# Optimization experiments

Measured on AMD Instinct MI355X. Metric: run time of the kernel, lower is better.

The kernel has to match this reference:

```python
import jax, jax.numpy as jnp
import numpy as np
from jax import lax

GROUPS = 8            # _resolve_groups(256, 8) == 8
EPS = 1e-5            # GroupNorm default eps
TOPK_RATIO = 0.2
MEAN_W, TOPK_W = 0.7, 0.3
DMG_THRESH = 0.5
DN = ('NCHW', 'OIHW', 'NCHW')


def _normalize(p, axis=1):
    # clamp_min(1e-8) / clamp_min(1e-8).sum().clamp_min(1e-8)
    p = jnp.maximum(p, 1e-8)
    return p / jnp.maximum(p.sum(axis=axis, keepdims=True), 1e-8)


def _conv_head(x, w1, gn_s, gn_b, w2, b2):
    # Conv3x3(no bias) -> GroupNorm(8) -> GELU(exact) -> Dropout(eval: identity) -> Conv1x1
    h = lax.conv_general_dilated(x, w1, (1, 1), 'SAME', dimension_numbers=DN)
    B, C, H, W = h.shape
    hg = h.reshape(B, GROUPS, C // GROUPS, H, W)
    mu = jnp.mean(hg, axis=(2, 3, 4), keepdims=True)
    var = jnp.var(hg, axis=(2, 3, 4), keepdims=True)
    h = ((hg - mu) * lax.rsqrt(var + EPS)).reshape(B, C, H, W)
    h = h * gn_s[None, :, None, None] + gn_b[None, :, None, None]
    h = jax.nn.gelu(h, approximate=False)
    return lax.conv_general_dilated(h, w2, (1, 1), 'SAME', dimension_numbers=DN) + b2[None, :, None, None]


def _forward(feature_map, target_mask, dw1, dgs, dgb, dw2, db2, sw1, sgs, sgb, sw2, sb2):
    dmg_logit = _conv_head(feature_map, dw1, dgs, dgb, dw2, db2)      # [B,1,H,W]
    corn_logits = _conv_head(feature_map, sw1, sgs, sgb, sw2, sb2)    # [B,2,H,W]

    # CORN dense decode: threshold probs = cumprod(sigmoid), classes = K+1
    t = jnp.cumprod(jax.nn.sigmoid(corn_logits), axis=1)              # [B,2,H,W]
    sev = jnp.concatenate([1.0 - t[:, :1], t[:, :-1] - t[:, 1:], t[:, -1:]], axis=1)  # [B,3,H,W]
    sev = _normalize(sev, axis=1)

    p_dmg = jax.nn.sigmoid(dmg_logit)                                 # [B,1,H,W]
    pix = jnp.concatenate([1.0 - p_dmg, p_dmg * sev], axis=1)         # [B,4,H,W]
    pix = _normalize(pix, axis=1)

    sev_pred = jnp.argmax(sev, axis=1) + 1                            # [B,H,W]
    pred_labels = jnp.where(p_dmg[:, 0] >= DMG_THRESH, sev_pred, 0)

    # target_mask already at feature resolution -> nearest resize is identity
    valid = target_mask > 0.5                                         # [B,1,H,W] bool
    B, C, H, W = pix.shape
    N = H * W
    flat = pix.transpose(0, 2, 3, 1).reshape(B, N, C)                 # [B,N,C]
    mf = valid.reshape(B, N)                                          # [B,N]
    cnt = mf.sum(axis=1)                                              # [B] int
    uniform = jnp.full((B, C), 1.0 / C, dtype=flat.dtype)

    # masked mean
    denom = jnp.maximum(cnt, 1).astype(flat.dtype)[:, None]
    mean_p = (flat * mf[..., None]).sum(axis=1) / denom
    mean_p = jnp.where((cnt == 0)[:, None], uniform, mean_p)
    mean_p = _normalize(mean_p, axis=1)

    # masked top-k mean via descending sort + cumsum gather (probs >= 0, invalid -> -1)
    masked = jnp.where(mf[..., None], flat, jnp.asarray(-1.0, flat.dtype))
    srt = -jnp.sort(-masked, axis=1)                                  # descending [B,N,C]
    csum = jnp.cumsum(srt, axis=1)
    k = jnp.clip(jnp.round(cnt.astype(jnp.float32) * TOPK_RATIO).astype(jnp.int32), 1, jnp.maximum(cnt, 1))
    idx = jnp.broadcast_to((k - 1)[:, None, None], (B, 1, C))
    topk_p = jnp.take_along_axis(csum, idx, axis=1)[:, 0] / k.astype(flat.dtype)[:, None]
    topk_p = jnp.where((cnt == 0)[:, None], uniform, topk_p)
    topk_p = _normalize(topk_p, axis=1)

    agg = _normalize(MEAN_W * mean_p + TOPK_W * topk_p, axis=1)
    agg_labels = jnp.argmax(agg, axis=1)

    return (dmg_logit, corn_logits, pix, pred_labels, mean_p, topk_p, agg, agg_labels)


def setup_inputs() -> dict:
    key = jax.random.key(0)
    ks = jax.random.split(key, 8)
    B, Cin, Ch, H, W = 8, 256, 256, 128, 128
    inp = {
        'feature_map': jax.random.normal(ks[0], (B, Cin, H, W), jnp.float32),
        'target_mask': jax.random.uniform(ks[1], (B, 1, H, W), jnp.float32),
        # damage head: Conv3x3 -> GN -> Conv1x1 (1 out)
        'dw1': jax.random.normal(ks[2], (Ch, Cin, 3, 3), jnp.float32) * 0.05,
        'dgs': jnp.ones((Ch,), jnp.float32),
        'dgb': jnp.zeros((Ch,), jnp.float32),
        'dw2': jax.random.normal(ks[3], (1, Ch, 1, 1), jnp.float32) * 0.05,
        'db2': jnp.zeros((1,), jnp.float32),
        # severity head: Conv3x3 -> GN -> Conv1x1 (2 thresholds)
        'sw1': jax.random.normal(ks[4], (Ch, Cin, 3, 3), jnp.float32) * 0.05,
        'sgs': jnp.ones((Ch,), jnp.float32),
        'sgb': jnp.zeros((Ch,), jnp.float32),
        'sw2': jax.random.normal(ks[5], (2, Ch, 1, 1), jnp.float32) * 0.05,
        'sb2': jnp.zeros((2,), jnp.float32),
    }
    return inp


def reference(feature_map, target_mask, dw1, dgs, dgb, dw2, db2, sw1, sgs, sgb, sw2, sb2):
    return _forward(feature_map, target_mask, dw1, dgs, dgb, dw2, db2, sw1, sgs, sgb, sw2, sb2)
```

## Files before the change

### kernel.cpp

```cpp
#include <hip/hip_runtime.h>
#include <hip/hip_bf16.h>

#define BB   8
#define CIN  256
#define CHN  256
#define HH   128
#define WWD  128
#define HW   (HH * WWD)
#define GRP_ELEMS ((size_t)32 * HW)

#define FLAG_DL   4e-3f
#define FLAG_GAP  1.5e-3f

#define BO_DSUM1   0
#define BO_DSUM2   1024
#define BO_FSTAT1  2048
#define BO_FSTAT2  2560
#define BO_DSTAT1  3072
#define BO_DSTAT2  4096
#define BO_MEAN    5120
#define BO_CNT     5248
#define BO_TOPK    5280
#define BO_FLAGC   5408
#define MEMSET_BYTES 8192
#define BO_WL      8192
#define WLCAP      32768

#define XP_OFF    139264ull
#define XP_BYTES  67108864ull
#define HB_OFF    (XP_OFF + XP_BYTES)
#define HB_BYTES  134217728ull
#define WH_OFF    (HB_OFF + HB_BYTES)
#define WT_BYTES  1179648ull
#define WL_OFF    (WH_OFF + WT_BYTES)
#define WT32_OFF  (WL_OFF + WT_BYTES)
#define WT32_BYTES 4718592ull
#define MFMA_NEED (WT32_OFF + WT32_BYTES)

#define O_DMG   0
#define O_CORN  131072
#define O_PIX   393216
#define O_LAB   917504
#define O_MEAN  1048576
#define O_TOPK  1048608
#define O_AGG   1048640
#define O_ALAB  1048672

typedef __attribute__((ext_vector_type(8))) _Float16 f16x8;
typedef __attribute__((ext_vector_type(4))) float f32x4;

__device__ inline ushort f2h(float f) {
    _Float16 h = (_Float16)f;
    union { _Float16 h; ushort u; } c; c.h = h; return c.u;
}
__device__ inline float h2f(ushort u) {
    union { ushort u; _Float16 h; } c; c.u = u; return (float)c.h;
}

__device__ inline void store4v(float* p, float a, float b, float c, float d) {
    *(float4*)p = make_float4(a, b, c, d);
}
__device__ inline void store4v(__hip_bfloat16* p, float a, float b, float c, float d) {
    p[0] = __float2bfloat16(a); p[1] = __float2bfloat16(b);
    p[2] = __float2bfloat16(c); p[3] = __float2bfloat16(d);
}
__device__ inline float ldv(const float* p) { return *p; }
__device__ inline float ldv(const __hip_bfloat16* p) { return __bfloat162float(*p); }


__global__ __launch_bounds__(256) void pack_x_f16(
    const float* __restrict__ x, ushort* __restrict__ Xh)
{
    int bid = blockIdx.x;
    int cc = bid & 7;
    int y  = (bid >> 3) & 127;
    int b  = bid >> 10;
    __shared__ ushort tile[32][132];
    for (int i = threadIdx.x; i < 4096; i += 256) {
        int ci = i >> 7, xx = i & 127;
        float v = x[(((size_t)b * 256 + cc * 32 + ci) * 128 + y) * 128 + xx];
        tile[ci][xx] = f2h(v);
    }
    __syncthreads();
    ushort* dst = Xh + ((((size_t)b * 128 + y) * 8 + cc) << 12);
    for (int i = threadIdx.x; i < 4096; i += 256) {
        int xx = i >> 5, ci = i & 31;
        dst[i] = tile[ci][xx];
    }
}

__global__ __launch_bounds__(256) void transpose_w(
    const float* __restrict__ w, ushort* __restrict__ Whh,
    ushort* __restrict__ Whl, float* __restrict__ Wt32)
{
    int idx = blockIdx.x * 256 + threadIdx.x;
    int tap = idx >> 16;
    int rem = idx & 65535;
    int cc  = rem >> 13;
    int co  = (rem >> 5) & 255;
    int ci5 = rem & 31;
    int ci  = cc * 32 + ci5;
    float v = w[((size_t)co * 256 + ci) * 9 + tap];
    ushort h = f2h(v);
    int sidx = (((tap * 8 + cc) * 16 + (co >> 4)) << 9)
             + (((co & 15) + ((ci5 >> 3) << 4)) << 3) + (ci5 & 7);
    Whh[sidx] = h;
    Whl[sidx] = f2h(v - h2f(h));
    Wt32[((size_t)tap * 256 + ci) * 256 + co] = v;
}

__device__ __forceinline__ void gld16(const void* g, void* l)
{
    __builtin_amdgcn_global_load_lds(
        (const __attribute__((address_space(1))) void*)g,
        (__attribute__((address_space(3))) void*)l, 16, 0, 0);
}

__device__ __forceinline__ void issue_b_slice(
    const ushort* __restrict__ Whh, const ushort* __restrict__ Whl,
    ushort* dst, int u, int co0, int tid, int wb)
{
    const int su  = u / 3;
    const int kxu = u - su * 3;
    const int tap = ((su >> 3) * 3) + kxu;
    const int cc  = su & 7;
    const size_t sbase = ((size_t)((tap * 8 + cc) * 16 + (co0 >> 4)) << 9);
    const ushort* s0 = Whh + sbase;
    const ushort* s1 = Whl + sbase;
#pragma unroll
    for (int k = 0; k < 2; k++)
        gld16(s0 + (k * 256 + tid) * 8, dst + (size_t)(k * 256 + wb) * 8);
#pragma unroll
    for (int k = 0; k < 2; k++)
        gld16(s1 + (k * 256 + tid) * 8, dst + 4096 + (size_t)(k * 256 + wb) * 8);
}

__device__ __forceinline__ void issue_a_slice(
    const ushort* __restrict__ Xh, const ushort* __restrict__ zb,
    ushort* dst, int b, int y, int sn, int tid, int wb)
{
    const int kyn = sn >> 3, ccn = sn & 7;
    const int rown = y + kyn - 1;
    const bool rv = (unsigned)rown < 128u;
    const ushort* base = rv ? (Xh + ((((size_t)b * 128 + rown) * 8 + ccn) << 12)) : zb;
#pragma unroll
    for (int k = 0; k < 2; k++) {
        int idx = k * 256 + tid;
        int xi  = (idx + 4) >> 2;
        int q   = (idx & 3) ^ ((xi >> 1) & 3);
        int off = rv ? ((xi - 1) * 32 + q * 8) : (idx * 8);
        gld16(base + off, dst + 32 + (size_t)(k * 256 + wb) * 8);
    }
}

__global__ __launch_bounds__(256, 3) void conv3x3_mfma(
    const ushort* __restrict__ Xh, const ushort* __restrict__ Whh,
    const ushort* __restrict__ Whl, const ushort* __restrict__ zb,
    float* __restrict__ hout, double* __restrict__ sums)
{
    __shared__ ushort a_lds[2][4160];
    __shared__ ushort b_lds[2][8192];
    __shared__ float sred[8];

    const int bx  = blockIdx.x;
    const int y   = bx & 127;
    const int b   = bx >> 7;
    const int co0 = blockIdx.y << 7;
    const int tid  = threadIdx.x;
    const int lane = tid & 63;
    const int wb   = tid & 192;
    const int wv   = tid >> 6;
    const int m = lane & 15;
    const int q = lane >> 4;
    const int wpx = (wv & 1) << 6;
    const int wco = (wv >> 1) << 6;
    const int g0  = wco >> 4;

    if (tid < 8) sred[tid] = 0.f;
    if (tid < 16) {
        int tg = tid >> 2, p4 = tid & 3;
        ushort* r = &a_lds[tg >> 1][(tg & 1) ? (129 * 32) : 0];
        *(uint4*)(r + p4 * 8) = make_uint4(0u, 0u, 0u, 0u);
    }

    f32x4 acc[4][4];
#pragma unroll
    for (int f = 0; f < 4; f++)
#pragma unroll
        for (int g = 0; g < 4; g++) acc[f][g] = (f32x4){0.f, 0.f, 0.f, 0.f};

    issue_a_slice(Xh, zb, a_lds[0], b, y, 0, tid, wb);
    issue_b_slice(Whh, Whl, b_lds[0], 0, co0, tid, wb);
    asm volatile("s_waitcnt lgkmcnt(0)" ::: "memory");

    for (int s = 0; s < 24; s++) {
        const ushort* acur = a_lds[s & 1];
#pragma unroll
        for (int kx = 0; kx < 3; kx++) {
            const int t = 3 * s + kx;
            asm volatile("" ::: "memory");
            __builtin_amdgcn_s_barrier();
            {
                int u = t + 1;
                int ub = u & 1;
                if (u > 71) u = 71;
                issue_b_slice(Whh, Whl, b_lds[ub], u, co0, tid, wb);
            }
            if (kx == 0) {
                int sn = s + 1;
                int ab = sn & 1;
                if (sn > 23) sn = 23;
                issue_a_slice(Xh, zb, a_lds[ab], b, y, sn, tid, wb);
            }
            if (kx == 2) asm volatile("s_waitcnt vmcnt(4)" ::: "memory");
            else         asm volatile("s_waitcnt vmcnt(6)" ::: "memory");
            __builtin_amdgcn_s_barrier();
            asm volatile("" ::: "memory");

            const ushort* bb = b_lds[t & 1];
            f16x8 ah[4], bh[4], bl[4];
#pragma unroll
            for (int f = 0; f < 4; f++) {
                int row = wpx + f * 16 + kx + m;
                ah[f] = *(const f16x8*)(acur + row * 32
                        + ((q ^ ((row >> 1) & 3)) << 3));
            }
#pragma unroll
            for (int g = 0; g < 4; g++) {
                int off = ((g0 + g) << 9) + (lane << 3);
                bh[g] = *(const f16x8*)&bb[off];
                bl[g] = *(const f16x8*)&bb[4096 + off];
            }
            __builtin_amdgcn_s_setprio(1);
#pragma unroll
            for (int f = 0; f < 4; f++)
#pragma unroll
                for (int g = 0; g < 4; g++)
                    acc[f][g] = __builtin_amdgcn_mfma_f32_16x16x32_f16(ah[f], bh[g], acc[f][g], 0, 0, 0);
#pragma unroll
            for (int f = 0; f < 4; f++)
#pragma unroll
                for (int g = 0; g < 4; g++)
                    acc[f][g] = __builtin_amdgcn_mfma_f32_16x16x32_f16(ah[f], bl[g], acc[f][g], 0, 0, 0);
            __builtin_amdgcn_s_setprio(0);
        }
    }

    float s0 = 0.f, q0 = 0.f, s1 = 0.f, q1 = 0.f;
#pragma unroll
    for (int f = 0; f < 4; f++) {
#pragma unroll
        for (int g = 0; g < 4; g++) {
            f32x4 v = acc[f][g];
            float a = v.x + v.y + v.z + v.w;
            float qq = v.x * v.x + v.y * v.y + v.z * v.z + v.w * v.w;
            if (g < 2) { s0 += a; q0 += qq; } else { s1 += a; q1 += qq; }
            int px = wpx + f * 16 + q * 4;
            int co = co0 + wco + g * 16 + m;
            *(f32x4*)&hout[((size_t)(b * 256 + co) * 128 + y) * 128 + px] = v;
        }
    }
    int gl = wco >> 5;
    atomicAdd(&sred[gl],     s0);
    atomicAdd(&sred[gl + 1], s1);
    atomicAdd(&sred[4 + gl],     q0);
    atomicAdd(&sred[4 + gl + 1], q1);
    __syncthreads();
    if (tid < 4) atomicAdd(&sums[b * 8 + (co0 >> 5) + tid], (double)sred[tid]);
    else if (tid < 8) atomicAdd(&sums[64 + b * 8 + (co0 >> 5) + tid - 4], (double)sred[tid]);
}

template <typename HT>
__global__ __launch_bounds__(256) void conv3x3_gn_stats(
    const float* __restrict__ x, const float* __restrict__ w,
    HT* __restrict__ hout, double* __restrict__ sums)
{
    __shared__ float in_lds[8][3][132];
    __shared__ float w_lds[8][9][68];
    __shared__ float sred[2], qred[2];

    const int bx  = blockIdx.x;
    const int y   = bx & (HH - 1);
    const int b   = bx >> 7;
    const int co0 = blockIdx.y << 6;
    const int tid = threadIdx.x;
    if (tid < 2) { sred[tid] = 0.f; qred[tid] = 0.f; }
    const int tco = (tid & 15) << 2;
    const int tox = (tid >> 4) << 3;

    float acc[4][8];
#pragma unroll
    for (int i = 0; i < 4; i++)
#pragma unroll
        for (int j = 0; j < 8; j++) acc[i][j] = 0.f;

    const float* xb = x + (size_t)b * CIN * HW;
    for (int c0 = 0; c0 < CIN; c0 += 8) {
        __syncthreads();
        for (int i = tid; i < 8 * 3 * 130; i += 256) {
            int ci  = i / 390;
            int rem = i - ci * 390;
            int r   = rem / 130;
            int cx  = rem - r * 130;
            int gy  = y + r - 1;
            int gx  = cx - 1;
            float v = 0.f;
            if ((unsigned)gy < HH && (unsigned)gx < WWD)
                v = xb[(size_t)(c0 + ci) * HW + gy * WWD + gx];
            in_lds[ci][r][cx] = v;
        }
        for (int i = tid; i < 64 * 72; i += 256) {
            int co = i / 72;
            int kk = i - co * 72;
            int ci = kk / 9;
            int k9 = kk - ci * 9;
            w_lds[ci][k9][co] = w[((size_t)(co0 + co) * CIN + (c0 + ci)) * 9 + k9];
        }
        __syncthreads();
#pragma unroll
        for (int ci = 0; ci < 8; ci++) {
#pragma unroll
            for (int ky = 0; ky < 3; ky++) {
                const float* rowp = &in_lds[ci][ky][tox];
                float4 a0 = *(const float4*)rowp;
                float4 a1 = *(const float4*)(rowp + 4);
                float2 a2 = *(const float2*)(rowp + 8);
                float in10[10] = {a0.x, a0.y, a0.z, a0.w,
                                  a1.x, a1.y, a1.z, a1.w, a2.x, a2.y};
#pragma unroll
                for (int kx = 0; kx < 3; kx++) {
                    float4 wv = *(const float4*)&w_lds[ci][ky * 3 + kx][tco];
#pragma unroll
                    for (int ox = 0; ox < 8; ox++) {
                        float iv = in10[ox + kx];
                        acc[0][ox] = fmaf(iv, wv.x, acc[0][ox]);
                        acc[1][ox] = fmaf(iv, wv.y, acc[1][ox]);
                        acc[2][ox] = fmaf(iv, wv.z, acc[2][ox]);
                        acc[3][ox] = fmaf(iv, wv.w, acc[3][ox]);
                    }
                }
            }
        }
    }

    float s = 0.f, qv = 0.f;
#pragma unroll
    for (int oc = 0; oc < 4; oc++)
#pragma unroll
        for (int ox = 0; ox < 8; ox++) { float v = acc[oc][ox]; s += v; qv = fmaf(v, v, qv); }
#pragma unroll
    for (int oc = 0; oc < 4; oc++) {
        size_t base = ((size_t)(b * CHN + co0 + tco + oc)) * HW + y * WWD + tox;
        store4v(hout + base,     acc[oc][0], acc[oc][1], acc[oc][2], acc[oc][3]);
        store4v(hout + base + 4, acc[oc][4], acc[oc][5], acc[oc][6], acc[oc][7]);
    }
    const int gsel = tco >> 5;
    atomicAdd(&sred[gsel], s);
    atomicAdd(&qred[gsel], qv);
    __syncthreads();
    if (tid < 2) {
        int grp = (co0 >> 5) + tid;
        atomicAdd(&sums[b * 8 + grp],      (double)sred[tid]);
        atomicAdd(&sums[64 + b * 8 + grp], (double)qred[tid]);
    }
}

__global__ void gn_finalize(const double* __restrict__ dsums,
                            float* __restrict__ fstats, double* __restrict__ dstats)
{
    int i = threadIdx.x;
    if (i < 64) {
        double inv = 1.0 / (double)GRP_ELEMS;
        double mu  = dsums[i] * inv;
        double ex2 = dsums[64 + i] * inv;
        double var = ex2 - mu * mu;
        double rs  = 1.0 / sqrt(var + 1e-5);
        fstats[i]      = (float)mu;
        fstats[64 + i] = (float)rs;
        dstats[i]      = mu;
        dstats[64 + i] = rs;
    }
}

template <typename HT>
__global__ __launch_bounds__(256) void gn_head(
    const HT* __restrict__ hbuf,
    const float* __restrict__ gs, const float* __restrict__ gb,
    const float* __restrict__ w2, const float* __restrict__ b2,
    const float* __restrict__ stats,
    float* __restrict__ out, int nout)
{
    __shared__ float sc[256], sh[256], w2s[2][256];
    const int b = blockIdx.y;
    const int p = blockIdx.x * 256 + threadIdx.x;
    {
        int c = threadIdx.x;
        float mu = stats[b * 8 + (c >> 5)];
        float rs = stats[64 + b * 8 + (c >> 5)];
        float s  = gs[c] * rs;
        sc[c] = s;
        sh[c] = gb[c] - mu * s;
        w2s[0][c] = w2[c];
        w2s[1][c] = (nout > 1) ? w2[256 + c] : 0.f;
    }
    __syncthreads();
    const HT* hp = hbuf + (size_t)b * CHN * HW + p;
    float a0 = 0.f, a1 = 0.f;
    for (int c = 0; c < 256; c++) {
        float v = ldv(hp + (size_t)c * HW);
        v = fmaf(v, sc[c], sh[c]);
        float g = 0.5f * v * (1.f + erff(v * 0.70710678118654752440f));
        a0 = fmaf(g, w2s[0][c], a0);
        a1 = fmaf(g, w2s[1][c], a1);
    }
    out[(size_t)b * nout * HW + p] = a0 + b2[0];
    if (nout > 1) out[(size_t)b * nout * HW + HW + p] = a1 + b2[1];
}

__global__ __launch_bounds__(256) void decode_kernel(
    float* __restrict__ outw, const float* __restrict__ mask,
    float* __restrict__ meanacc, float* __restrict__ cntacc,
    int* __restrict__ flagcnt, int* __restrict__ wl)
{
    const int b = blockIdx.y;
    const int p = blockIdx.x * 256 + threadIdx.x;

    float dl = outw[O_DMG + b * HW + p];
    float c0 = outw[O_CORN + (b * 2 + 0) * HW + p];
    float c1 = outw[O_CORN + (b * 2 + 1) * HW + p];

    float s0 = 1.f / (1.f + expf(-c0));
    float s1 = 1.f / (1.f + expf(-c1));
    float t0 = s0, t1 = s0 * s1;
    float e0 = fmaxf(1.f - t0, 1e-8f);
    float e1 = fmaxf(t0 - t1, 1e-8f);
    float e2 = fmaxf(t1, 1e-8f);
    float es = fmaxf(e0 + e1 + e2, 1e-8f);
    e0 /= es; e1 /= es; e2 /= es;

    float pd = 1.f / (1.f + expf(-dl));
    float q0 = fmaxf(1.f - pd, 1e-8f);
    float q1 = fmaxf(pd * e0, 1e-8f);
    float q2 = fmaxf(pd * e1, 1e-8f);
    float q3 = fmaxf(pd * e2, 1e-8f);
    float qs = fmaxf(q0 + q1 + q2 + q3, 1e-8f);
    q0 /= qs; q1 /= qs; q2 /= qs; q3 /= qs;

    outw[O_PIX + ((size_t)b * 4 + 0) * HW + p] = q0;
    outw[O_PIX + ((size_t)b * 4 + 1) * HW + p] = q1;
    outw[O_PIX + ((size_t)b * 4 + 2) * HW + p] = q2;
    outw[O_PIX + ((size_t)b * 4 + 3) * HW + p] = q3;

    int am = 0; float bv = e0;
    if (e1 > bv) { bv = e1; am = 1; }
    if (e2 > bv) { bv = e2; am = 2; }
    outw[O_LAB + b * HW + p] = (pd >= 0.5f) ? (float)(am + 1) : 0.f;

    bool flag = (fabsf(dl) < FLAG_DL);
    {
        float top1 = e0, top2 = fmaxf(e1, e2);
        if (e1 > top1) { top1 = e1; top2 = fmaxf(e0, e2); }
        if (e2 > top1) { top1 = e2; top2 = fmaxf(e0, e1); }
        if ((top1 - top2 < FLAG_GAP) && (dl > -FLAG_DL)) flag = true;
    }
    if (flag) {
        int idx = atomicAdd(flagcnt, 1);
        if (idx < WLCAP) wl[idx] = b * HW + p;
    }

    bool valid = mask[b * HW + p] > 0.5f;
    float vm = valid ? 1.f : 0.f;
    float v0 = valid ? q0 : 0.f, v1 = valid ? q1 : 0.f;
    float v2 = valid ? q2 : 0.f, v3 = valid ? q3 : 0.f;

#pragma unroll
    for (int o = 32; o; o >>= 1) {
        v0 += __shfl_down(v0, o); v1 += __shfl_down(v1, o);
        v2 += __shfl_down(v2, o); v3 += __shfl_down(v3, o);
        vm += __shfl_down(vm, o);
    }
    __shared__ float racc[5];
    if (threadIdx.x < 5) racc[threadIdx.x] = 0.f;
    __syncthreads();
    if ((threadIdx.x & 63) == 0) {
        atomicAdd(&racc[0], v0); atomicAdd(&racc[1], v1);
        atomicAdd(&racc[2], v2); atomicAdd(&racc[3], v3);
        atomicAdd(&racc[4], vm);
    }
    __syncthreads();
    if (threadIdx.x < 4) atomicAdd(&meanacc[b * 4 + threadIdx.x], racc[threadIdx.x]);
    if (threadIdx.x == 4) atomicAdd(&cntacc[b], racc[4]);
}

__global__ __launch_bounds__(256) void fixup_labels(
    const float* __restrict__ x, const float* __restrict__ Wt32,
    const float* __restrict__ dgs, const float* __restrict__ dgb,
    const float* __restrict__ dw2, const float* __restrict__ db2,
    const float* __restrict__ sgs, const float* __restrict__ sgb,
    const float* __restrict__ sw2, const float* __restrict__ sb2,
    const double* __restrict__ dstat1, const double* __restrict__ dstat2,
    const int* __restrict__ wl, const int* __restrict__ wcnt,
    float* __restrict__ out)
{
    __shared__ float xp[2304];
    __shared__ double dpart[4][256];
    __shared__ double wred[3][4];

    int count = *wcnt;
    if (count > WLCAP) count = WLCAP;
    const int tid  = threadIdx.x;
    const int lane = tid & 63;
    const int wv   = tid >> 6;
    const int c4   = lane << 2;
    const int j0   = wv * 576;

    for (int pix = blockIdx.x; pix < count; pix += gridDim.x) {
        __syncthreads();
        const int pid = wl[pix];
        const int b = pid >> 14, yy = (pid >> 7) & 127, xx = pid & 127;
        for (int i = tid; i < 2304; i += 256) {
            int t = i >> 8, ci = i & 255;
            int ky = t / 3, kx = t - ky * 3;
            int gy = yy + ky - 1, gx = xx + kx - 1;
            float v = 0.f;
            if ((unsigned)gy < 128u && (unsigned)gx < 128u)
                v = x[(((size_t)b * 256 + ci) * 128 + gy) * 128 + gx];
            xp[i] = v;
        }
        __syncthreads();

        for (int head = 0; head < 2; head++) {
            const float* gs  = head ? sgs : dgs;
            const float* gb  = head ? sgb : dgb;
            const float* w2  = head ? sw2 : dw2;
            const double* st = head ? dstat2 : dstat1;
            const float* wt  = Wt32 + (size_t)head * 589824;

            double a0 = 0.0, a1 = 0.0, a2 = 0.0, a3 = 0.0;
            for (int jc = 0; jc < 576; jc += 8) {
                float4 wv4[8];
#pragma unroll
                for (int u = 0; u < 8; u++)
                    wv4[u] = *(const float4*)&wt[(size_t)(j0 + jc + u) * 256 + c4];
#pragma unroll
                for (int u = 0; u < 8; u++) {
                    double xv = (double)xp[j0 + jc + u];
                    a0 += xv * (double)wv4[u].x;
                    a1 += xv * (double)wv4[u].y;
                    a2 += xv * (double)wv4[u].z;
                    a3 += xv * (double)wv4[u].w;
                }
            }
            dpart[wv][c4]     = a0;
            dpart[wv][c4 + 1] = a1;
            dpart[wv][c4 + 2] = a2;
            dpart[wv][c4 + 3] = a3;
            __syncthreads();

            {
                const int c = tid;
                double h = dpart[0][c] + dpart[1][c] + dpart[2][c] + dpart[3][c];
                double mu = st[b * 8 + (c >> 5)];
                double rs = st[64 + b * 8 + (c >> 5)];
                double v = (h - mu) * rs * (double)gs[c] + (double)gb[c];
                double g = 0.5 * v * (1.0 + erf(v * 0.70710678118654752440));
                double r0 = g * (double)w2[c];
#pragma unroll
                for (int o = 32; o; o >>= 1) r0 += __shfl_down(r0, o);
                if (lane == 0) wred[head][wv] = r0;
                if (head == 1) {
                    double r1 = g * (double)w2[256 + c];
#pragma unroll
                    for (int o = 32; o; o >>= 1) r1 += __shfl_down(r1, o);
                    if (lane == 0) wred[2][wv] = r1;
                }
            }
            __syncthreads();
        }

        if (tid == 0) {
            double dlv = wred[0][0] + wred[0][1] + wred[0][2] + wred[0][3] + (double)db2[0];
            double c0v = wred[1][0] + wred[1][1] + wred[1][2] + wred[1][3] + (double)sb2[0];
            double c1v = wred[2][0] + wred[2][1] + wred[2][2] + wred[2][3] + (double)sb2[1];
            double s0 = 1.0 / (1.0 + exp(-c0v));
            double s1 = 1.0 / (1.0 + exp(-c1v));
            double t0 = s0, t1 = s0 * s1;
            double e0 = fmax(1.0 - t0, 1e-8);
            double e1 = fmax(t0 - t1, 1e-8);
            double e2 = fmax(t1, 1e-8);
            int am = 0; double bv = e0;
            if (e1 > bv) { bv = e1; am = 1; }
            if (e2 > bv) { bv = e2; am = 2; }
            out[O_LAB + pid] = (dlv >= 0.0) ? (float)(am + 1) : 0.f;
        }
    }
}

__global__ __launch_bounds__(256) void topk_kernel(
    const float* __restrict__ outw, const float* __restrict__ mask,
    const float* __restrict__ cntacc, float* __restrict__ topkout)
{
    const int b = blockIdx.x >> 2;
    const int c = blockIdx.x & 3;
    const int tid = threadIdx.x;

    __shared__ int hist[256];
    __shared__ unsigned s_prefix;
    __shared__ int s_want;
    __shared__ float s_red[4];
    __shared__ int s_redi[4];

    float cntf = cntacc[b];
    int cnt = (int)cntf;
    int k = (int)rintf(cntf * 0.2f);
    if (k < 1) k = 1;
    int kmax = cnt > 1 ? cnt : 1;
    if (k > kmax) k = kmax;

    if (tid == 0) { s_prefix = 0u; s_want = k; }

    const float* pv = outw + O_PIX + ((size_t)b * 4 + c) * HW;
    const float* pm = mask + (size_t)b * HW;

    for (int pass = 0; pass < 4; pass++) {
        hist[tid] = 0;
        __syncthreads();
        const int shift = 24 - 8 * pass;
        const unsigned pmask = pass ? (0xFFFFFFFFu << (shift + 8)) : 0u;
        const unsigned prefix = s_prefix;
        for (int p = tid; p < HW; p += 256) {
            float v = (pm[p] > 0.5f) ? pv[p] : -1.0f;
            unsigned bits = __float_as_uint(v);
            unsigned u = (bits & 0x80000000u) ? ~bits : (bits | 0x80000000u);
            if ((u & pmask) == prefix) atomicAdd(&hist[(u >> shift) & 255], 1);
        }
        __syncthreads();
        if (tid == 0) {
            int want = s_want;
            int bin = 255;
            while (bin > 0) {
                int h = hist[bin];
                if (want <= h) break;
                want -= h;
                bin--;
            }
            s_want = want;
            s_prefix = prefix | ((unsigned)bin << shift);
        }
        __syncthreads();
    }
    const unsigned tau = s_prefix;

    float sgt = 0.f; int cgt = 0;
    for (int p = tid; p < HW; p += 256) {
        float v = (pm[p] > 0.5f) ? pv[p] : -1.0f;
        unsigned bits = __float_as_uint(v);
        unsigned u = (bits & 0x80000000u) ? ~bits : (bits | 0x80000000u);
        if (u > tau) { sgt += v; cgt++; }
    }
#pragma unroll
    for (int o = 32; o; o >>= 1) { sgt += __shfl_down(sgt, o); cgt += __shfl_down(cgt, o); }
    if ((tid & 63) == 0) { s_red[tid >> 6] = sgt; s_redi[tid >> 6] = cgt; }
    __syncthreads();
    if (tid == 0) {
        float S = s_red[0] + s_red[1] + s_red[2] + s_red[3];
        int   C = s_redi[0] + s_redi[1] + s_redi[2] + s_redi[3];
        unsigned tb = (tau & 0x80000000u) ? (tau & 0x7FFFFFFFu) : ~tau;
        float tf = __uint_as_float(tb);
        float total = S + (float)(k - C) * tf;
        topkout[b * 4 + c] = total / (float)k;
    }
}

__device__ inline void norm4(float* p)
{
    float a = fmaxf(p[0], 1e-8f), b = fmaxf(p[1], 1e-8f);
    float c = fmaxf(p[2], 1e-8f), d = fmaxf(p[3], 1e-8f);
    float s = fmaxf(a + b + c + d, 1e-8f);
    p[0] = a / s; p[1] = b / s; p[2] = c / s; p[3] = d / s;
}

__global__ void final_kernel(const float* __restrict__ meanacc,
                             const float* __restrict__ cntacc,
                             const float* __restrict__ topkv,
                             float* __restrict__ outw)
{
    int b = threadIdx.x;
    if (b >= 8) return;
    float cnt = cntacc[b];
    bool zero = (cnt == 0.f);
    float denom = fmaxf(cnt, 1.f);
    float m[4], t[4], a[4];
#pragma unroll
    for (int c = 0; c < 4; c++) {
        m[c] = zero ? 0.25f : meanacc[b * 4 + c] / denom;
        t[c] = zero ? 0.25f : topkv[b * 4 + c];
    }
    norm4(m); norm4(t);
#pragma unroll
    for (int c = 0; c < 4; c++) a[c] = 0.7f * m[c] + 0.3f * t[c];
    norm4(a);
    int am = 0; float bv = a[0];
#pragma unroll
    for (int c = 1; c < 4; c++) if (a[c] > bv) { bv = a[c]; am = c; }
#pragma unroll
    for (int c = 0; c < 4; c++) {
        outw[O_MEAN + b * 4 + c] = m[c];
        outw[O_TOPK + b * 4 + c] = t[c];
        outw[O_AGG  + b * 4 + c] = a[c];
    }
    outw[O_ALAB + b] = (float)am;
}

extern "C" void kernel_launch(void* const* d_in, const int* in_sizes, int n_in,
                              void* d_out, int out_size, void* d_ws, size_t ws_size,
                              hipStream_t stream)
{
    (void)in_sizes; (void)n_in; (void)out_size;
    const float* x    = (const float*)d_in[0];
    const float* mask = (const float*)d_in[1];
    const float* dw1  = (const float*)d_in[2];
    const float* dgs  = (const float*)d_in[3];
    const float* dgb  = (const float*)d_in[4];
    const float* dw2  = (const float*)d_in[5];
    const float* db2  = (const float*)d_in[6];
    const float* sw1  = (const float*)d_in[7];
    const float* sgs  = (const float*)d_in[8];
    const float* sgb  = (const float*)d_in[9];
    const float* sw2  = (const float*)d_in[10];
    const float* sb2  = (const float*)d_in[11];
    float* out = (float*)d_out;

    char* wsb = (char*)d_ws;
    double* dsum1  = (double*)(wsb + BO_DSUM1);
    double* dsum2  = (double*)(wsb + BO_DSUM2);
    float*  fstat1 = (float*)(wsb + BO_FSTAT1);
    float*  fstat2 = (float*)(wsb + BO_FSTAT2);
    double* dstat1 = (double*)(wsb + BO_DSTAT1);
    double* dstat2 = (double*)(wsb + BO_DSTAT2);
    float*  meanacc = (float*)(wsb + BO_MEAN);
    float*  cntacc  = (float*)(wsb + BO_CNT);
    float*  topkv   = (float*)(wsb + BO_TOPK);
    int*    flagc   = (int*)(wsb + BO_FLAGC);
    int*    wl      = (int*)(wsb + BO_WL);

    hipMemsetAsync(d_ws, 0, MEMSET_BYTES + 8192, stream);

    dim3 pgrid(64, BB);

    if (ws_size >= MFMA_NEED) {
        ushort* Xh   = (ushort*)(wsb + XP_OFF);
        float*  hb   = (float*)(wsb + HB_OFF);
        ushort* Whh  = (ushort*)(wsb + WH_OFF);
        ushort* Whl  = (ushort*)(wsb + WL_OFF);
        float*  Wt32 = (float*)(wsb + WT32_OFF);
        const ushort* zb = (const ushort*)(wsb + BO_WL);

        pack_x_f16<<<8192, 256, 0, stream>>>(x, Xh);

        dim3 cgrid(1024, 2);
        transpose_w<<<2304, 256, 0, stream>>>(dw1, Whh, Whl, Wt32);
        conv3x3_mfma<<<cgrid, 256, 0, stream>>>(Xh, Whh, Whl, zb, hb, dsum1);
        gn_finalize<<<1, 64, 0, stream>>>(dsum1, fstat1, dstat1);
        gn_head<float><<<pgrid, 256, 0, stream>>>(hb, dgs, dgb, dw2, db2,
                                                  fstat1, out + O_DMG, 1);
        transpose_w<<<2304, 256, 0, stream>>>(sw1, Whh, Whl, Wt32 + 589824);
        conv3x3_mfma<<<cgrid, 256, 0, stream>>>(Xh, Whh, Whl, zb, hb, dsum2);
        gn_finalize<<<1, 64, 0, stream>>>(dsum2, fstat2, dstat2);
        gn_head<float><<<pgrid, 256, 0, stream>>>(hb, sgs, sgb, sw2, sb2,
                                                  fstat2, out + O_CORN, 2);

        decode_kernel<<<pgrid, 256, 0, stream>>>(out, mask, meanacc, cntacc, flagc, wl);
        fixup_labels<<<512, 256, 0, stream>>>(x, Wt32, dgs, dgb, dw2, db2,
                                              sgs, sgb, sw2, sb2,
                                              dstat1, dstat2, wl, flagc, out);
        topk_kernel<<<32, 256, 0, stream>>>(out, mask, cntacc, topkv);
        final_kernel<<<1, 64, 0, stream>>>(meanacc, cntacc, topkv, out);
    } else {
        void* hbuf = wsb + XP_OFF;
        dim3 cgrid(HH * BB, CHN / 64);
        const size_t needF32 = XP_OFF + (size_t)BB * CHN * HW * sizeof(float);
        if (ws_size >= needF32) {
            conv3x3_gn_stats<float><<<cgrid, 256, 0, stream>>>(x, dw1, (float*)hbuf, dsum1);
            gn_finalize<<<1, 64, 0, stream>>>(dsum1, fstat1, dstat1);
            gn_head<float><<<pgrid, 256, 0, stream>>>((float*)hbuf, dgs, dgb, dw2, db2,
                                                      fstat1, out + O_DMG, 1);
            conv3x3_gn_stats<float><<<cgrid, 256, 0, stream>>>(x, sw1, (float*)hbuf, dsum2);
            gn_finalize<<<1, 64, 0, stream>>>(dsum2, fstat2, dstat2);
            gn_head<float><<<pgrid, 256, 0, stream>>>((float*)hbuf, sgs, sgb, sw2, sb2,
                                                      fstat2, out + O_CORN, 2);
        } else {
            conv3x3_gn_stats<__hip_bfloat16><<<cgrid, 256, 0, stream>>>(x, dw1, (__hip_bfloat16*)hbuf, dsum1);
            gn_finalize<<<1, 64, 0, stream>>>(dsum1, fstat1, dstat1);
            gn_head<__hip_bfloat16><<<pgrid, 256, 0, stream>>>((__hip_bfloat16*)hbuf, dgs, dgb, dw2, db2,
                                                               fstat1, out + O_DMG, 1);
            conv3x3_gn_stats<__hip_bfloat16><<<cgrid, 256, 0, stream>>>(x, sw1, (__hip_bfloat16*)hbuf, dsum2);
            gn_finalize<<<1, 64, 0, stream>>>(dsum2, fstat2, dstat2);
            gn_head<__hip_bfloat16><<<pgrid, 256, 0, stream>>>((__hip_bfloat16*)hbuf, sgs, sgb, sw2, sb2,
                                                               fstat2, out + O_CORN, 2);
        }
        decode_kernel<<<pgrid, 256, 0, stream>>>(out, mask, meanacc, cntacc, flagc, wl);
        topk_kernel<<<32, 256, 0, stream>>>(out, mask, cntacc, topkv);
        final_kernel<<<1, 64, 0, stream>>>(meanacc, cntacc, topkv, out);
    }
}
```

Baseline: 1.318 ms.

## Vectorize packing, coalesce weight transpose, reorder conv grid, cache top-k values in registers

Several unrelated changes land together. The input pack now uses float4 loads and 16-byte stores. The weight transpose stages through shared memory so the fp32 transposed write is coalesced. The conv block index mapping is swapped so consecutive blocks cover different batches at the same row. The GELU projection loop is unrolled, and the top-k radix select loads each thread's 64 values into registers once instead of re-reading global memory on every pass. The main conv kernel dominates the runtime and only changes its block order, so the overall gain is likely small. The 64-entry register array in top-k raises register pressure.

```diff
diff --git a/kernel.cpp b/kernel.cpp
--- a/kernel.cpp
+++ b/kernel.cpp
@@ -75,17 +75,26 @@
     int cc = bid & 7;
     int y  = (bid >> 3) & 127;
     int b  = bid >> 10;
-    __shared__ ushort tile[32][132];
-    for (int i = threadIdx.x; i < 4096; i += 256) {
-        int ci = i >> 7, xx = i & 127;
-        float v = x[(((size_t)b * 256 + cc * 32 + ci) * 128 + y) * 128 + xx];
-        tile[ci][xx] = f2h(v);
+    __shared__ ushort tile[32][137];
+    const int tid = threadIdx.x;
+    for (int i = tid; i < 1024; i += 256) {
+        int ci = i >> 5;
+        int x4 = (i & 31) << 2;
+        float4 v = *(const float4*)&x[(((size_t)b * 256 + cc * 32 + ci) * 128 + y) * 128 + x4];
+        tile[ci][x4 + 0] = f2h(v.x);
+        tile[ci][x4 + 1] = f2h(v.y);
+        tile[ci][x4 + 2] = f2h(v.z);
+        tile[ci][x4 + 3] = f2h(v.w);
     }
     __syncthreads();
     ushort* dst = Xh + ((((size_t)b * 128 + y) * 8 + cc) << 12);
-    for (int i = threadIdx.x; i < 4096; i += 256) {
-        int xx = i >> 5, ci = i & 31;
-        dst[i] = tile[ci][xx];
+    for (int i = tid; i < 512; i += 256) {
+        int xx  = i >> 2;
+        int ci0 = (i & 3) << 3;
+        ushort tmp[8];
+#pragma unroll
+        for (int j = 0; j < 8; j++) tmp[j] = tile[ci0 + j][xx];
+        *(uint4*)&dst[i << 3] = *(uint4*)tmp;
     }
 }
 
@@ -93,6 +102,7 @@
     const float* __restrict__ w, ushort* __restrict__ Whh,
     ushort* __restrict__ Whl, float* __restrict__ Wt32)
 {
+    __shared__ float lt[8][33];
     int idx = blockIdx.x * 256 + threadIdx.x;
     int tap = idx >> 16;
     int rem = idx & 65535;
@@ -106,7 +116,12 @@
              + (((co & 15) + ((ci5 >> 3) << 4)) << 3) + (ci5 & 7);
     Whh[sidx] = h;
     Whl[sidx] = f2h(v - h2f(h));
-    Wt32[((size_t)tap * 256 + ci) * 256 + co] = v;
+    lt[threadIdx.x >> 5][ci5] = v;
+    __syncthreads();
+    int co_base = (blockIdx.x * 8) & 255;
+    int ci5w = threadIdx.x >> 3;
+    int j    = threadIdx.x & 7;
+    Wt32[((size_t)tap * 256 + cc * 32 + ci5w) * 256 + co_base + j] = lt[j][ci5w];
 }
 
 __device__ __forceinline__ void gld16(const void* g, void* l)
@@ -162,9 +177,9 @@
     __shared__ ushort b_lds[2][8192];
     __shared__ float sred[8];
 
-    const int bx  = blockIdx.x;
-    const int y   = bx & 127;
-    const int b   = bx >> 7;
+    const int bxr = blockIdx.x;
+    const int y   = bxr >> 3;
+    const int b   = bxr & 7;
     const int co0 = blockIdx.y << 7;
     const int tid  = threadIdx.x;
     const int lane = tid & 63;
@@ -406,6 +421,7 @@
     __syncthreads();
     const HT* hp = hbuf + (size_t)b * CHN * HW + p;
     float a0 = 0.f, a1 = 0.f;
+#pragma unroll 4
     for (int c = 0; c < 256; c++) {
         float v = ldv(hp + (size_t)c * HW);
         v = fmaf(v, sc[c], sh[c]);
@@ -622,16 +638,24 @@
     const float* pv = outw + O_PIX + ((size_t)b * 4 + c) * HW;
     const float* pm = mask + (size_t)b * HW;
 
+    unsigned uv[64];
+#pragma unroll
+    for (int j = 0; j < 64; j++) {
+        int p = tid + (j << 8);
+        float v = (pm[p] > 0.5f) ? pv[p] : -1.0f;
+        unsigned bits = __float_as_uint(v);
+        uv[j] = (bits & 0x80000000u) ? ~bits : (bits | 0x80000000u);
+    }
+
     for (int pass = 0; pass < 4; pass++) {
         hist[tid] = 0;
         __syncthreads();
         const int shift = 24 - 8 * pass;
         const unsigned pmask = pass ? (0xFFFFFFFFu << (shift + 8)) : 0u;
         const unsigned prefix = s_prefix;
-        for (int p = tid; p < HW; p += 256) {
-            float v = (pm[p] > 0.5f) ? pv[p] : -1.0f;
-            unsigned bits = __float_as_uint(v);
-            unsigned u = (bits & 0x80000000u) ? ~bits : (bits | 0x80000000u);
+#pragma unroll
+        for (int j = 0; j < 64; j++) {
+            unsigned u = uv[j];
             if ((u & pmask) == prefix) atomicAdd(&hist[(u >> shift) & 255], 1);
         }
         __syncthreads();
@@ -652,11 +676,14 @@
     const unsigned tau = s_prefix;
 
     float sgt = 0.f; int cgt = 0;
-    for (int p = tid; p < HW; p += 256) {
-        float v = (pm[p] > 0.5f) ? pv[p] : -1.0f;
-        unsigned bits = __float_as_uint(v);
-        unsigned u = (bits & 0x80000000u) ? ~bits : (bits | 0x80000000u);
-        if (u > tau) { sgt += v; cgt++; }
+#pragma unroll
+    for (int j = 0; j < 64; j++) {
+        unsigned u = uv[j];
+        if (u > tau) {
+            unsigned bits = (u & 0x80000000u) ? (u & 0x7FFFFFFFu) : ~u;
+            sgt += __uint_as_float(bits);
+            cgt++;
+        }
     }
 #pragma unroll
     for (int o = 32; o; o >>= 1) { sgt += __shfl_down(sgt, o); cgt += __shfl_down(cgt, o); }
```

Result: faster. 1.260 ms (-4.4%).
